# Performance work log

Hardware: AMD Instinct MI355X
Metric: run time of the kernel (lower is better)

## Reference

```python
import jax, jax.numpy as jnp
import numpy as np

B, T, D = 4, 512, 192
CLAMP = 1e20


def setup_inputs() -> dict:
    key = jax.random.key(0)
    k1, k2 = jax.random.split(key, 2)
    x = jax.random.normal(k1, (B, T, D), dtype=jnp.float32)
    W = jax.random.normal(k2, (3 * D, D), dtype=jnp.float32) * 0.02  # c_attn weight
    b = jnp.zeros((3 * D,), dtype=jnp.float32)                       # c_attn bias
    S0 = jnp.zeros((B, 1, D, D), dtype=jnp.float32)                  # recurrent state S
    Z0 = jnp.zeros((B, 1, D), dtype=jnp.float32)                     # recurrent state Z
    return {"x": x, "W": W, "b": b, "S0": S0, "Z0": Z0}


def reference(x, W, b, S0, Z0):
    # c_attn: Linear(d_model -> 3*d_model), split into Q, K, V
    qkv = x @ W.T + b
    Q, K, V = jnp.split(qkv, 3, axis=2)
    # Phi: elu(x) + 1 feature map on Q and K
    Q = jax.nn.elu(Q) + 1.0
    K = jax.nn.elu(K) + 1.0

    # outer-product state: S[b,t] = clamp(cumsum_t K_t V_t^T) + S0
    outer = jnp.einsum('bti,btj->btij', K, V)                 # [B,T,D,D]
    S = jnp.clip(jnp.cumsum(outer, axis=1), -CLAMP, CLAMP) + S0
    Z = jnp.clip(jnp.cumsum(K, axis=1), -CLAMP, CLAMP) + Z0   # [B,T,D]

    numerator = jnp.einsum('bti,btil->btl', Q, S)             # [B,T,D]
    denominator = jnp.einsum('bti,bti->bt', Q, Z)[..., None] + 1e-5
    output = numerator / denominator

    Bz, Tz, F = K.shape
    S_last = S[:, -1].reshape(Bz, F * F)
    Z_last = Z[:, -1]
    return output, S_last, Z_last
```

## Files before the change

### kernel.cpp

```cpp
#include <hip/hip_runtime.h>
#include <cmath>

#define TB  512
#define DD  192
#define NCH 8
#define CKL 64

static __device__ __forceinline__ float elu1(float v) {
    return v > 0.0f ? v + 1.0f : expf(v);
}

__global__ __launch_bounds__(256) void k_qkv(
    const float* __restrict__ x, const float* __restrict__ W,
    const float* __restrict__ bias,
    float* __restrict__ Qp, float* __restrict__ Kp, float* __restrict__ Vp)
{
    __shared__ float xs[32][68];
    __shared__ float wsT[64 * 64];
    const int tid = threadIdx.x;
    const int n0 = blockIdx.x * 32;
    const int m0 = blockIdx.y * 64;
    const int a  = tid >> 4;
    const int c  = tid & 15;

    float acc[2][4];
    #pragma unroll
    for (int r = 0; r < 2; ++r)
        #pragma unroll
        for (int s = 0; s < 4; ++s) acc[r][s] = 0.f;

    for (int kb = 0; kb < DD; kb += 64) {
        #pragma unroll
        for (int p = 0; p < 2; ++p) {
            int q = p * 256 + tid;
            int row = q >> 4, c4 = (q & 15) * 4;
            *(float4*)&xs[row][c4] = *(const float4*)&x[(n0 + row) * DD + kb + c4];
        }
        #pragma unroll
        for (int p = 0; p < 4; ++p) {
            int q = p * 256 + tid;
            int mrow = q >> 4, kidx = q & 15;
            float4 wv = *(const float4*)&W[(m0 + mrow) * DD + kb + kidx * 4];
            int g = (mrow >> 2) ^ kidx;
            int pcol = g * 4 + (mrow & 3);
            wsT[(kidx * 4 + 0) * 64 + pcol] = wv.x;
            wsT[(kidx * 4 + 1) * 64 + pcol] = wv.y;
            wsT[(kidx * 4 + 2) * 64 + pcol] = wv.z;
            wsT[(kidx * 4 + 3) * 64 + pcol] = wv.w;
        }
        __syncthreads();
        #pragma unroll
        for (int kk = 0; kk < 64; kk += 4) {
            float4 xv0 = *(const float4*)&xs[a][kk];
            float4 xv1 = *(const float4*)&xs[16 + a][kk];
            const int g = (c ^ ((kk >> 2) & 15)) * 4;
            float x0[4] = {xv0.x, xv0.y, xv0.z, xv0.w};
            float x1[4] = {xv1.x, xv1.y, xv1.z, xv1.w};
            #pragma unroll
            for (int j = 0; j < 4; ++j) {
                float4 wk = *(const float4*)&wsT[(kk + j) * 64 + g];
                acc[0][0] += x0[j] * wk.x; acc[0][1] += x0[j] * wk.y;
                acc[0][2] += x0[j] * wk.z; acc[0][3] += x0[j] * wk.w;
                acc[1][0] += x1[j] * wk.x; acc[1][1] += x1[j] * wk.y;
                acc[1][2] += x1[j] * wk.z; acc[1][3] += x1[j] * wk.w;
            }
        }
        __syncthreads();
    }

    const int reg  = m0 / DD;
    float* dst = (reg == 0) ? Qp : (reg == 1 ? Kp : Vp);
    const int mloc = (m0 % DD) + c * 4;
    #pragma unroll
    for (int r = 0; r < 2; ++r) {
        int n = n0 + r * 16 + a;
        float v0 = acc[r][0] + bias[m0 + c * 4 + 0];
        float v1 = acc[r][1] + bias[m0 + c * 4 + 1];
        float v2 = acc[r][2] + bias[m0 + c * 4 + 2];
        float v3 = acc[r][3] + bias[m0 + c * 4 + 3];
        if (reg < 2) { v0 = elu1(v0); v1 = elu1(v1); v2 = elu1(v2); v3 = elu1(v3); }
        *(float4*)&dst[n * DD + mloc] = make_float4(v0, v1, v2, v3);
    }
}

__global__ __launch_bounds__(256) void k_mid(
    const float* __restrict__ Kp, const float* __restrict__ Vp,
    const float* __restrict__ Qp,
    float* __restrict__ Mws, float* __restrict__ zws,
    float* __restrict__ Aws, float* __restrict__ denws)
{
    __shared__ float sm[64 * 196 + 16 * 196];
    const int tid  = threadIdx.x;
    const int bc   = blockIdx.x;
    const int role = blockIdx.y;
    const int base = bc * CKL;

    if (role < 6) {
        const int ih = role / 3, jh = role % 3;
        float (*Ks)[100] = (float (*)[100])sm;
        float (*Vs)[68]  = (float (*)[68])(sm + 6400);

        #pragma unroll
        for (int p = 0; p < 6; ++p) {
            int q = p * 256 + tid;
            int row = q / 24, c4 = (q % 24) * 4;
            *(float4*)&Ks[row][c4] = *(const float4*)&Kp[(base + row) * DD + ih * 96 + c4];
        }
        #pragma unroll
        for (int p = 0; p < 4; ++p) {
            int q = p * 256 + tid;
            int row = q >> 4, c4 = (q & 15) * 4;
            *(float4*)&Vs[row][c4] = *(const float4*)&Vp[(base + row) * DD + jh * 64 + c4];
        }
        __syncthreads();

        const int ig = tid >> 4, jg = tid & 15;
        const int iL = ig * 6;
        float acc[6][4];
        #pragma unroll
        for (int i = 0; i < 6; ++i)
            #pragma unroll
            for (int j = 0; j < 4; ++j) acc[i][j] = 0.f;

        #pragma unroll 4
        for (int t = 0; t < CKL; ++t) {
            float4 v = *(const float4*)&Vs[t][jg * 4];
            float2 k0 = *(const float2*)&Ks[t][iL + 0];
            float2 k1 = *(const float2*)&Ks[t][iL + 2];
            float2 k2 = *(const float2*)&Ks[t][iL + 4];
            float kv[6] = {k0.x, k0.y, k1.x, k1.y, k2.x, k2.y};
            #pragma unroll
            for (int i = 0; i < 6; ++i) {
                acc[i][0] += kv[i] * v.x;
                acc[i][1] += kv[i] * v.y;
                acc[i][2] += kv[i] * v.z;
                acc[i][3] += kv[i] * v.w;
            }
        }

        float* Mout = Mws + (size_t)bc * DD * DD;
        const int j0 = jh * 64 + jg * 4;
        #pragma unroll
        for (int i = 0; i < 6; ++i)
            *(float4*)&Mout[(ih * 96 + iL + i) * DD + j0] =
                make_float4(acc[i][0], acc[i][1], acc[i][2], acc[i][3]);

        if (jh == 0 && tid < 96) {
            float s = 0.f;
            #pragma unroll 8
            for (int t = 0; t < CKL; ++t) s += Ks[t][tid];
            zws[bc * DD + ih * 96 + tid] = s;
        }
    } else {
        const int tq = role - 6;
        const int tbase = tq * 16;
        float (*Ks)[196] = (float (*)[196])sm;
        float (*Qs)[196] = (float (*)[196])(sm + 64 * 196);

        #pragma unroll
        for (int p = 0; p < 12; ++p) {
            int q = p * 256 + tid;
            int row = q / 48, c4 = (q % 48) * 4;
            *(float4*)&Ks[row][c4] = *(const float4*)&Kp[(base + row) * DD + c4];
        }
        #pragma unroll
        for (int p = 0; p < 3; ++p) {
            int q = p * 256 + tid;
            int row = q / 48, c4 = (q % 48) * 4;
            *(float4*)&Qs[row][c4] = *(const float4*)&Qp[(base + tbase + row) * DD + c4];
        }
        __syncthreads();

        const int trow = tid >> 4, tc = tid & 15;
        const int tg = tbase + trow;
        float acc[4];
        #pragma unroll
        for (int s = 0; s < 4; ++s) acc[s] = 0.f;

        #pragma unroll 4
        for (int k = 0; k < DD; k += 4) {
            float4 qv = *(const float4*)&Qs[trow][k];
            #pragma unroll
            for (int s = 0; s < 4; ++s) {
                float4 kv = *(const float4*)&Ks[tc * 4 + s][k];
                acc[s] += qv.x*kv.x + qv.y*kv.y + qv.z*kv.z + qv.w*kv.w;
            }
        }

        float av[4], psum = 0.f;
        #pragma unroll
        for (int s = 0; s < 4; ++s) {
            int tau = tc * 4 + s;
            av[s] = (tau <= tg) ? acc[s] : 0.f;
            psum += av[s];
        }
        *(float4*)&Aws[bc * 4096 + tg * 64 + tc * 4] =
            make_float4(av[0], av[1], av[2], av[3]);
        #pragma unroll
        for (int off = 1; off < 16; off <<= 1)
            psum += __shfl_xor(psum, off, 16);
        if (tc == 0) denws[base + tg] = psum;
    }
}

__global__ __launch_bounds__(256) void k_out(
    const float* __restrict__ Qp, const float* __restrict__ Vp,
    const float* __restrict__ Aws, const float* __restrict__ denws,
    const float* __restrict__ Mws, const float* __restrict__ zws,
    const float* __restrict__ S0, const float* __restrict__ Z0,
    float* __restrict__ out, float* __restrict__ Slast, float* __restrict__ Zlast)
{
    __shared__ float As[64][68];
    __shared__ float Ss[DD][16];
    __shared__ float Vs[CKL][16];
    __shared__ float Zs[DD];
    const int tid = threadIdx.x;
    const int bc  = blockIdx.x;
    const int lq  = blockIdx.y;
    const int b   = bc >> 3, c = bc & 7;
    const int base = bc * CKL;
    const int lofs = lq * 16;

    #pragma unroll
    for (int p = 0; p < 4; ++p) {
        int q = p * 256 + tid;
        int row = q >> 4, c4 = (q & 15) * 4;
        *(float4*)&As[row][c4] = *(const float4*)&Aws[bc * 4096 + row * 64 + c4];
    }
    {
        int row = tid >> 2, c4 = (tid & 3) * 4;
        *(float4*)&Vs[row][c4] = *(const float4*)&Vp[(base + row) * DD + lofs + c4];
    }
    {
        float4 r[3];
        #pragma unroll
        for (int p = 0; p < 3; ++p) {
            int q = p * 256 + tid;
            int row = q >> 2, c4 = (q & 3) * 4;
            r[p] = *(const float4*)&S0[(size_t)b * DD * DD + row * DD + lofs + c4];
        }
        for (int cc = 0; cc < c; ++cc) {
            const float* Mc = Mws + (size_t)(b * NCH + cc) * DD * DD;
            #pragma unroll
            for (int p = 0; p < 3; ++p) {
                int q = p * 256 + tid;
                int row = q >> 2, c4 = (q & 3) * 4;
                float4 m = *(const float4*)&Mc[row * DD + lofs + c4];
                r[p].x += m.x; r[p].y += m.y; r[p].z += m.z; r[p].w += m.w;
            }
        }
        #pragma unroll
        for (int p = 0; p < 3; ++p) {
            int q = p * 256 + tid;
            int row = q >> 2, c4 = (q & 3) * 4;
            *(float4*)&Ss[row][c4] = r[p];
        }
        if (c == NCH - 1) {
            const float* M7 = Mws + (size_t)(b * NCH + 7) * DD * DD;
            #pragma unroll
            for (int p = 0; p < 3; ++p) {
                int q = p * 256 + tid;
                int row = q >> 2, c4 = (q & 3) * 4;
                float4 m = *(const float4*)&M7[row * DD + lofs + c4];
                *(float4*)&Slast[(size_t)b * DD * DD + row * DD + lofs + c4] =
                    make_float4(r[p].x + m.x, r[p].y + m.y, r[p].z + m.z, r[p].w + m.w);
            }
        }
    }
    if (tid < DD) {
        float z = Z0[b * DD + tid];
        for (int cc = 0; cc < c; ++cc)
            z += zws[(b * NCH + cc) * DD + tid];
        Zs[tid] = z;
        if (c == NCH - 1 && lq == 0)
            Zlast[b * DD + tid] = z + zws[(b * NCH + 7) * DD + tid];
    }
    __syncthreads();

    const int t  = tid >> 2;
    const int lg = (tid & 3) * 4;
    float ax = 0.f, ay = 0.f, az = 0.f, aw = 0.f, dacc = 0.f;

    #pragma unroll 16
    for (int tau = 0; tau < CKL; ++tau) {
        float a = As[t][tau];
        float4 v = *(const float4*)&Vs[tau][lg];
        ax += a * v.x; ay += a * v.y; az += a * v.z; aw += a * v.w;
    }

    const float* Qrow = Qp + (size_t)(base + t) * DD;
    #pragma unroll 4
    for (int i = 0; i < DD; i += 4) {
        float4 qv = *(const float4*)&Qrow[i];
        float qq[4] = {qv.x, qv.y, qv.z, qv.w};
        #pragma unroll
        for (int u = 0; u < 4; ++u) {
            float4 s = *(const float4*)&Ss[i + u][lg];
            ax += qq[u] * s.x; ay += qq[u] * s.y;
            az += qq[u] * s.z; aw += qq[u] * s.w;
            dacc += qq[u] * Zs[i + u];
        }
    }

    float den = denws[base + t] + dacc + 1e-5f;
    float inv = 1.f / den;
    *(float4*)&out[(size_t)(base + t) * DD + lofs + lg] =
        make_float4(ax * inv, ay * inv, az * inv, aw * inv);
}

extern "C" void kernel_launch(void* const* d_in, const int* in_sizes, int n_in,
                              void* d_out, int out_size, void* d_ws, size_t ws_size,
                              hipStream_t stream)
{
    const float* x  = (const float*)d_in[0];
    const float* W  = (const float*)d_in[1];
    const float* bb = (const float*)d_in[2];
    const float* S0 = (const float*)d_in[3];
    const float* Z0 = (const float*)d_in[4];

    float* out   = (float*)d_out;
    float* Slast = out + (size_t)4 * TB * DD;
    float* Zlast = Slast + (size_t)4 * DD * DD;

    float* ws   = (float*)d_ws;
    float* Qp   = ws;
    float* Kp   = Qp + (size_t)4 * TB * DD;
    float* Vp   = Kp + (size_t)4 * TB * DD;
    float* Mws  = Vp + (size_t)4 * TB * DD;
    float* zws  = Mws + (size_t)4 * NCH * DD * DD;
    float* Aws  = zws + (size_t)4 * NCH * DD;
    float* denw = Aws + (size_t)4 * NCH * CKL * CKL;

    k_qkv<<<dim3(64, 9),  256, 0, stream>>>(x, W, bb, Qp, Kp, Vp);
    k_mid<<<dim3(32, 10), 256, 0, stream>>>(Kp, Vp, Qp, Mws, zws, Aws, denw);
    k_out<<<dim3(32, 12), 256, 0, stream>>>(Qp, Vp, Aws, denw, Mws, zws,
                                            S0, Z0, out, Slast, Zlast);
}
```

Before: 102.2 us.

## Use bf16 MFMA for QKV projection and vectorize Z dot in output kernel

```diff
diff --git a/kernel.cpp b/kernel.cpp
--- a/kernel.cpp
+++ b/kernel.cpp
@@ -8,6 +8,16 @@
 
 static __device__ __forceinline__ float elu1(float v) {
     return v > 0.0f ? v + 1.0f : expf(v);
+}
+
+typedef __attribute__((ext_vector_type(8))) __bf16 bf16x8;
+typedef __attribute__((ext_vector_type(4))) float floatx4;
+
+static __device__ __forceinline__ __bf16 f2bf(float f) {
+    unsigned u = __builtin_bit_cast(unsigned, f);
+    u += 0x7FFF + ((u >> 16) & 1);
+    unsigned short h = (unsigned short)(u >> 16);
+    return __builtin_bit_cast(__bf16, h);
 }
 
 __global__ __launch_bounds__(256) void k_qkv(
@@ -15,71 +25,69 @@
     const float* __restrict__ bias,
     float* __restrict__ Qp, float* __restrict__ Kp, float* __restrict__ Vp)
 {
-    __shared__ float xs[32][68];
-    __shared__ float wsT[64 * 64];
+    __shared__ __bf16 xs[64][200];
+    __shared__ __bf16 wsb[64][200];
     const int tid = threadIdx.x;
-    const int n0 = blockIdx.x * 32;
+    const int n0 = blockIdx.x * 64;
     const int m0 = blockIdx.y * 64;
-    const int a  = tid >> 4;
-    const int c  = tid & 15;
-
-    float acc[2][4];
-    #pragma unroll
-    for (int r = 0; r < 2; ++r)
-        #pragma unroll
-        for (int s = 0; s < 4; ++s) acc[r][s] = 0.f;
-
-    for (int kb = 0; kb < DD; kb += 64) {
-        #pragma unroll
-        for (int p = 0; p < 2; ++p) {
-            int q = p * 256 + tid;
-            int row = q >> 4, c4 = (q & 15) * 4;
-            *(float4*)&xs[row][c4] = *(const float4*)&x[(n0 + row) * DD + kb + c4];
-        }
-        #pragma unroll
-        for (int p = 0; p < 4; ++p) {
-            int q = p * 256 + tid;
-            int mrow = q >> 4, kidx = q & 15;
-            float4 wv = *(const float4*)&W[(m0 + mrow) * DD + kb + kidx * 4];
-            int g = (mrow >> 2) ^ kidx;
-            int pcol = g * 4 + (mrow & 3);
-            wsT[(kidx * 4 + 0) * 64 + pcol] = wv.x;
-            wsT[(kidx * 4 + 1) * 64 + pcol] = wv.y;
-            wsT[(kidx * 4 + 2) * 64 + pcol] = wv.z;
-            wsT[(kidx * 4 + 3) * 64 + pcol] = wv.w;
-        }
-        __syncthreads();
-        #pragma unroll
-        for (int kk = 0; kk < 64; kk += 4) {
-            float4 xv0 = *(const float4*)&xs[a][kk];
-            float4 xv1 = *(const float4*)&xs[16 + a][kk];
-            const int g = (c ^ ((kk >> 2) & 15)) * 4;
-            float x0[4] = {xv0.x, xv0.y, xv0.z, xv0.w};
-            float x1[4] = {xv1.x, xv1.y, xv1.z, xv1.w};
-            #pragma unroll
-            for (int j = 0; j < 4; ++j) {
-                float4 wk = *(const float4*)&wsT[(kk + j) * 64 + g];
-                acc[0][0] += x0[j] * wk.x; acc[0][1] += x0[j] * wk.y;
-                acc[0][2] += x0[j] * wk.z; acc[0][3] += x0[j] * wk.w;
-                acc[1][0] += x1[j] * wk.x; acc[1][1] += x1[j] * wk.y;
-                acc[1][2] += x1[j] * wk.z; acc[1][3] += x1[j] * wk.w;
-            }
-        }
-        __syncthreads();
+
+    #pragma unroll
+    for (int p = 0; p < 12; ++p) {
+        int q = p * 256 + tid;
+        int row = q / 48, c4 = (q % 48) * 4;
+        float4 xv = *(const float4*)&x[(n0 + row) * DD + c4];
+        xs[row][c4 + 0] = f2bf(xv.x); xs[row][c4 + 1] = f2bf(xv.y);
+        xs[row][c4 + 2] = f2bf(xv.z); xs[row][c4 + 3] = f2bf(xv.w);
+        float4 wv = *(const float4*)&W[(m0 + row) * DD + c4];
+        wsb[row][c4 + 0] = f2bf(wv.x); wsb[row][c4 + 1] = f2bf(wv.y);
+        wsb[row][c4 + 2] = f2bf(wv.z); wsb[row][c4 + 3] = f2bf(wv.w);
+    }
+    __syncthreads();
+
+    const int wv_  = tid >> 6;
+    const int nh   = (wv_ & 1) * 32;
+    const int mh   = (wv_ >> 1) * 32;
+    const int lane = tid & 63;
+    const int r16  = lane & 15;
+    const int quad = lane >> 4;
+
+    floatx4 acc[2][2];
+    #pragma unroll
+    for (int tn = 0; tn < 2; ++tn)
+        #pragma unroll
+        for (int tm = 0; tm < 2; ++tm)
+            acc[tn][tm] = (floatx4){0.f, 0.f, 0.f, 0.f};
+
+    #pragma unroll
+    for (int ks = 0; ks < 6; ++ks) {
+        const int k0 = ks * 32 + quad * 8;
+        bf16x8 a0 = *(const bf16x8*)&xs[nh + 0  + r16][k0];
+        bf16x8 a1 = *(const bf16x8*)&xs[nh + 16 + r16][k0];
+        bf16x8 b0 = *(const bf16x8*)&wsb[mh + 0  + r16][k0];
+        bf16x8 b1 = *(const bf16x8*)&wsb[mh + 16 + r16][k0];
+        acc[0][0] = __builtin_amdgcn_mfma_f32_16x16x32_bf16(a0, b0, acc[0][0], 0, 0, 0);
+        acc[0][1] = __builtin_amdgcn_mfma_f32_16x16x32_bf16(a0, b1, acc[0][1], 0, 0, 0);
+        acc[1][0] = __builtin_amdgcn_mfma_f32_16x16x32_bf16(a1, b0, acc[1][0], 0, 0, 0);
+        acc[1][1] = __builtin_amdgcn_mfma_f32_16x16x32_bf16(a1, b1, acc[1][1], 0, 0, 0);
     }
 
     const int reg  = m0 / DD;
     float* dst = (reg == 0) ? Qp : (reg == 1 ? Kp : Vp);
-    const int mloc = (m0 % DD) + c * 4;
-    #pragma unroll
-    for (int r = 0; r < 2; ++r) {
-        int n = n0 + r * 16 + a;
-        float v0 = acc[r][0] + bias[m0 + c * 4 + 0];
-        float v1 = acc[r][1] + bias[m0 + c * 4 + 1];
-        float v2 = acc[r][2] + bias[m0 + c * 4 + 2];
-        float v3 = acc[r][3] + bias[m0 + c * 4 + 3];
-        if (reg < 2) { v0 = elu1(v0); v1 = elu1(v1); v2 = elu1(v2); v3 = elu1(v3); }
-        *(float4*)&dst[n * DD + mloc] = make_float4(v0, v1, v2, v3);
+    const int mbase = m0 % DD;
+    #pragma unroll
+    for (int tn = 0; tn < 2; ++tn) {
+        #pragma unroll
+        for (int tm = 0; tm < 2; ++tm) {
+            const int mloc = mh + tm * 16 + r16;
+            const float bs = bias[m0 + mloc];
+            #pragma unroll
+            for (int j = 0; j < 4; ++j) {
+                const int nloc = nh + tn * 16 + quad * 4 + j;
+                float v = acc[tn][tm][j] + bs;
+                if (reg < 2) v = elu1(v);
+                dst[(size_t)(n0 + nloc) * DD + mbase + mloc] = v;
+            }
+        }
     }
 }
 
@@ -213,7 +221,7 @@
     __shared__ float As[64][68];
     __shared__ float Ss[DD][16];
     __shared__ float Vs[CKL][16];
-    __shared__ float Zs[DD];
+    __shared__ __align__(16) float Zs[DD];
     const int tid = threadIdx.x;
     const int bc  = blockIdx.x;
     const int lq  = blockIdx.y;
@@ -292,13 +300,14 @@
     #pragma unroll 4
     for (int i = 0; i < DD; i += 4) {
         float4 qv = *(const float4*)&Qrow[i];
+        float4 zv = *(const float4*)&Zs[i];
+        dacc += qv.x*zv.x + qv.y*zv.y + qv.z*zv.z + qv.w*zv.w;
         float qq[4] = {qv.x, qv.y, qv.z, qv.w};
         #pragma unroll
         for (int u = 0; u < 4; ++u) {
             float4 s = *(const float4*)&Ss[i + u][lg];
             ax += qq[u] * s.x; ay += qq[u] * s.y;
             az += qq[u] * s.z; aw += qq[u] * s.w;
-            dacc += qq[u] * Zs[i + u];
         }
     }
 
@@ -331,7 +340,7 @@
     float* Aws  = zws + (size_t)4 * NCH * DD;
     float* denw = Aws + (size_t)4 * NCH * CKL * CKL;
 
-    k_qkv<<<dim3(64, 9),  256, 0, stream>>>(x, W, bb, Qp, Kp, Vp);
+    k_qkv<<<dim3(32, 9),  256, 0, stream>>>(x, W, bb, Qp, Kp, Vp);
     k_mid<<<dim3(32, 10), 256, 0, stream>>>(Kp, Vp, Qp, Mws, zws, Aws, denw);
     k_out<<<dim3(32, 12), 256, 0, stream>>>(Qp, Vp, Aws, denw, Mws, zws,
                                             S0, Z0, out, Slast, Zlast);
```

New measurement: 95.26 us. -6.8%, faster.
